# Kernel optimization log

Measured on AMD Instinct MI355X. Metric: run time of the kernel, lower is better.

The kernel has to match this reference:

```python
import jax, jax.numpy as jnp
import numpy as np

B, T, C, H, W = 2, 8, 512, 32, 32
HEADS, HD = 8, 64          # head_dim = C // num_heads
GROUPS = 32                # GroupNorm_0 num_groups
EPS = 1e-6


def setup_inputs() -> dict:
    key = jax.random.key(0)
    k = jax.random.split(key, 5)
    return {
        "x": jax.random.normal(k[0], (B, T, C, H, W), jnp.float32),
        "gn_scale": jnp.ones((C,), jnp.float32),
        "gn_bias": jnp.zeros((C,), jnp.float32),
        "w_qkv": jax.random.normal(k[1], (C, 3 * C), jnp.float32) / float(np.sqrt(C)),
        "b_qkv": jnp.zeros((3 * C,), jnp.float32),
        "w_out": jax.random.normal(k[2], (C, C), jnp.float32) / float(np.sqrt(C)),
        "b_out": jnp.zeros((C,), jnp.float32),
    }


def reference(x, gn_scale, gn_bias, w_qkv, b_qkv, w_out, b_out):
    Bv, Tv, Cv, Hv, Wv = x.shape
    N = Bv * Tv
    xv = x.reshape(N, Cv, Hv, Wv)

    # GroupNorm(32 groups, eps=1e-6) with affine
    g = xv.reshape(N, GROUPS, Cv // GROUPS, Hv, Wv)
    mu = g.mean(axis=(2, 3, 4), keepdims=True)
    var = g.var(axis=(2, 3, 4), keepdims=True)
    hn = ((g - mu) * jax.lax.rsqrt(var + EPS)).reshape(N, Cv, Hv, Wv)
    hn = hn * gn_scale[None, :, None, None] + gn_bias[None, :, None, None]

    # NIN qkv projection (per-pixel 1x1): (N,C,H,W) x (C,3C) -> (N,3C,H,W)
    h = jnp.einsum('nchw,cd->ndhw', hn, w_qkv) + b_qkv[None, :, None, None]
    h = h.reshape(N, HEADS, 3 * HD, Hv * Wv).transpose(0, 1, 3, 2)  # (N,h,S,3d)
    q, k, v = jnp.split(h, 3, axis=-1)

    # naive scaled dot-product attention over S = H*W tokens
    logits = jnp.einsum('nhsd,nhtd->nhst', q, k) / float(np.sqrt(HD))
    attn = jax.nn.softmax(logits, axis=-1)
    vals = jnp.einsum('nhst,nhtd->nhsd', attn, v)

    h = vals.transpose(0, 1, 3, 2).reshape(N, Cv, Hv, Wv)
    # output NIN (init_scale=0 in torch; random params here) + residual
    h = jnp.einsum('nchw,cd->ndhw', h, w_out) + b_out[None, :, None, None]
    return x + h.reshape(Bv, Tv, Cv, Hv, Wv)
```

## Files before the change

kernel.cpp:

```cpp
#include <hip/hip_runtime.h>
#include <stdint.h>

typedef __bf16 bf16x8 __attribute__((ext_vector_type(8)));
typedef float f32x4v __attribute__((ext_vector_type(4)));
typedef float f32x16v __attribute__((ext_vector_type(16)));
typedef unsigned u32x2 __attribute__((ext_vector_type(2)));

__device__ __forceinline__ unsigned f2bf_rn(float f) {
    return (__float_as_uint(f) + 0x8000u) >> 16;
}
__device__ __forceinline__ unsigned pk2bf(float a, float b) {
    return __builtin_amdgcn_perm(__float_as_uint(b) + 0x8000u,
                                 __float_as_uint(a) + 0x8000u, 0x07060302u);
}
__device__ __forceinline__ unsigned pk2bf_rne(float a, float b) {
    union { __bf16 h[2]; unsigned u; } x;
    x.h[0] = (__bf16)a; x.h[1] = (__bf16)b;
    return x.u;
}
__device__ __forceinline__ float fexp2(float x) {
#if __has_builtin(__builtin_amdgcn_exp2f)
    return __builtin_amdgcn_exp2f(x);
#else
    float r; asm volatile("v_exp_f32 %0, %1" : "=v"(r) : "v"(x)); return r;
#endif
}
__device__ __forceinline__ float frcp(float x) {
#if __has_builtin(__builtin_amdgcn_rcpf)
    return __builtin_amdgcn_rcpf(x);
#else
    float r; asm volatile("v_rcp_f32 %0, %1" : "=v"(r) : "v"(x)); return r;
#endif
}

__device__ __forceinline__ void swap32(unsigned &a, unsigned &b) {
#if __has_builtin(__builtin_amdgcn_permlane32_swap)
    u32x2 r = __builtin_amdgcn_permlane32_swap(a, b, false, false);
    a = r[0]; b = r[1];
#else
    unsigned pa = (unsigned)__shfl_xor((int)a, 32);
    unsigned pb = (unsigned)__shfl_xor((int)b, 32);
    bool hi = (threadIdx.x & 32) != 0;
    unsigned na = hi ? pb : a;
    unsigned nb = hi ? b : pa;
    a = na; b = nb;
#endif
}

__device__ __forceinline__ bf16x8 mk8(unsigned a, unsigned b, unsigned c, unsigned e) {
    union { int4 i; bf16x8 v; } u;
    u.i = make_int4((int)a, (int)b, (int)c, (int)e);
    return u.v;
}

#define GLD_LDS16(gp, lp) __builtin_amdgcn_global_load_lds( \
    (const __attribute__((address_space(1))) unsigned int*)(gp), \
    (__attribute__((address_space(3))) unsigned int*)(lp), 16, 0, 0)

__global__ __launch_bounds__(256) void wt_kernel(const float* __restrict__ wqkv,
        const float* __restrict__ wout, unsigned short* __restrict__ WqT,
        unsigned short* __restrict__ WoT) {
    __shared__ float tile[32][33];
    int bx = blockIdx.x;
    const float* in; unsigned short* out; int Cc, c0;
    if (bx < 48) { in = wqkv; out = WqT; Cc = 1536; c0 = bx * 32; }
    else         { in = wout; out = WoT; Cc = 512;  c0 = (bx - 48) * 32; }
    int r0 = blockIdx.y * 32;
    int tx = threadIdx.x & 31, ty = threadIdx.x >> 5;
    #pragma unroll
    for (int i = 0; i < 4; i++) {
        int r = ty + i * 8;
        tile[r][tx] = in[(size_t)(r0 + r) * Cc + c0 + tx];
    }
    __syncthreads();
    #pragma unroll
    for (int i = 0; i < 4; i++) {
        int cr = ty + i * 8;
        out[(size_t)(c0 + cr) * 512 + r0 + tx] = (unsigned short)f2bf_rn(tile[tx][cr]);
    }
}

__global__ __launch_bounds__(256) void gn_kernel(const float* __restrict__ x,
        const float* __restrict__ scale, const float* __restrict__ bias,
        unsigned short* __restrict__ hnT) {
    int blk = blockIdx.x;
    int tid = threadIdx.x;
    int g = blk & 31, n = blk >> 5;
    const float4* src4 = (const float4*)(x + (size_t)blk * 16384);

    __shared__ float xs[16][1028];
    float s = 0.f, s2 = 0.f;
    #pragma unroll
    for (int k = 0; k < 16; k++) {
        int i = tid + k * 256;
        float4 v = src4[i];
        int c = i >> 8, p4 = (i & 255) * 4;
        *(float4*)&xs[c][p4] = v;
        s  += v.x + v.y + v.z + v.w;
        s2 += v.x*v.x + v.y*v.y + v.z*v.z + v.w*v.w;
    }
    __shared__ float red[256], red2[256];
    red[tid] = s; red2[tid] = s2;
    __syncthreads();
    for (int off = 128; off > 0; off >>= 1) {
        if (tid < off) { red[tid] += red[tid+off]; red2[tid] += red2[tid+off]; }
        __syncthreads();
    }
    __shared__ float sc_s[16], bi_s[16];
    if (tid < 16) {
        float mean = red[0] * (1.f/16384.f);
        float var  = red2[0] * (1.f/16384.f) - mean*mean;
        float rstd = rsqrtf(var + 1e-6f);
        int c = g*16 + tid;
        float sc = scale[c] * rstd;
        sc_s[tid] = sc;
        bi_s[tid] = bias[c] - mean * sc;
    }
    __syncthreads();
    #pragma unroll
    for (int ch = 0; ch < 4; ch++) {
        int sQ = ch*256 + tid;
        unsigned int pk[8];
        #pragma unroll
        for (int c2 = 0; c2 < 8; c2++) {
            float a = xs[c2*2][sQ]   * sc_s[c2*2]   + bi_s[c2*2];
            float b = xs[c2*2+1][sQ] * sc_s[c2*2+1] + bi_s[c2*2+1];
            pk[c2] = pk2bf(a, b);
        }
        unsigned short* op = hnT + ((size_t)(n*1024 + sQ))*512 + g*16;
        *(uint4*)op       = make_uint4(pk[0], pk[1], pk[2], pk[3]);
        *((uint4*)op + 1) = make_uint4(pk[4], pk[5], pk[6], pk[7]);
    }
}

__global__ __launch_bounds__(256) void qkv_kernel(
        const unsigned short* __restrict__ WqT, const unsigned short* __restrict__ hnT,
        const float* __restrict__ bqkv,
        unsigned short* __restrict__ qb, unsigned short* __restrict__ kbuf,
        unsigned short* __restrict__ vb) {
    int s0 = blockIdx.x * 128, m0 = blockIdx.y * 128, n = blockIdx.z;
    __shared__ unsigned short At[8192];
    __shared__ unsigned short Bt[8192];
    int tid = threadIdx.x;
    int lane = tid & 63, w = tid >> 6;
    int quad = lane >> 4, tx = lane & 15;
    int moff = (w & 1) * 64, soff = (w >> 1) * 64;

    const unsigned short* Arow = WqT + (size_t)m0 * 512;
    const unsigned short* Brow = hnT + ((size_t)n * 1024 + s0) * 512;

    f32x4v acc[4][4];
    #pragma unroll
    for (int i = 0; i < 4; i++)
        #pragma unroll
        for (int j = 0; j < 4; j++)
            #pragma unroll
            for (int e = 0; e < 4; e++) acc[i][j][e] = 0.f;

    int f1 = tid, f2 = tid + 256;
    int m1 = f1 >> 2, kb1 = ((f1 & 3) - (f1 >> 3)) & 3;
    int m2 = f2 >> 2, kb2 = ((f2 & 3) - (f2 >> 3)) & 3;

    for (int k0 = 0; k0 < 512; k0 += 64) {
        __syncthreads();
        GLD_LDS16(Arow + (size_t)m1*512 + k0 + kb1*8,      At + f1*8);
        GLD_LDS16(Arow + (size_t)m2*512 + k0 + kb2*8,      At + f2*8);
        GLD_LDS16(Arow + (size_t)m1*512 + k0 + 32 + kb1*8, At + 4096 + f1*8);
        GLD_LDS16(Arow + (size_t)m2*512 + k0 + 32 + kb2*8, At + 4096 + f2*8);
        GLD_LDS16(Brow + (size_t)m1*512 + k0 + kb1*8,      Bt + f1*8);
        GLD_LDS16(Brow + (size_t)m2*512 + k0 + kb2*8,      Bt + f2*8);
        GLD_LDS16(Brow + (size_t)m1*512 + k0 + 32 + kb1*8, Bt + 4096 + f1*8);
        GLD_LDS16(Brow + (size_t)m2*512 + k0 + 32 + kb2*8, Bt + 4096 + f2*8);
        __syncthreads();
        #pragma unroll
        for (int kk = 0; kk < 2; kk++) {
            const unsigned short* Ab = At + kk*4096;
            const unsigned short* Bb = Bt + kk*4096;
            bf16x8 af[4], bfr[4];
            #pragma unroll
            for (int mt = 0; mt < 4; mt++) {
                int m = moff + mt*16 + tx;
                int ch = m*4 + ((quad + (m >> 1)) & 3);
                af[mt] = *(const bf16x8*)(Ab + ch*8);
            }
            #pragma unroll
            for (int nt = 0; nt < 4; nt++) {
                int m = soff + nt*16 + tx;
                int ch = m*4 + ((quad + (m >> 1)) & 3);
                bfr[nt] = *(const bf16x8*)(Bb + ch*8);
            }
            #pragma unroll
            for (int mt = 0; mt < 4; mt++)
                #pragma unroll
                for (int nt = 0; nt < 4; nt++)
                    acc[mt][nt] = __builtin_amdgcn_mfma_f32_16x16x32_bf16(
                        af[mt], bfr[nt], acc[mt][nt], 0, 0, 0);
        }
    }

    const float QSCL = 0.18033688011112042f;
    #pragma unroll
    for (int mt = 0; mt < 4; mt++) {
        int m = m0 + moff + mt*16 + quad*4;
        int head = m / 192;
        int r = m - head*192;
        int which = r >> 6;
        int d0 = r & 63;
        float4 bia = *(const float4*)(bqkv + m);
        float scl = (which == 0) ? QSCL : 1.0f;
        #pragma unroll
        for (int nt = 0; nt < 4; nt++) {
            int sQ = s0 + soff + nt*16 + tx;
            f32x4v a = acc[mt][nt];
            float v0 = (a[0]+bia.x)*scl, v1 = (a[1]+bia.y)*scl;
            float v2 = (a[2]+bia.z)*scl, v3 = (a[3]+bia.w)*scl;
            if (which < 2) {
                unsigned short* base = (which == 0) ? qb : kbuf;
                unsigned lo = pk2bf(v0, v1), hi2 = pk2bf(v2, v3);
                *(uint2*)(base + (((size_t)(n*8 + head)*1024 + sQ) << 6) + d0) =
                    make_uint2(lo, hi2);
            } else {
                size_t vbase = ((size_t)(n*8 + head)*64 + d0)*1024 + sQ;
                vb[vbase]        = (unsigned short)f2bf_rn(v0);
                vb[vbase + 1024] = (unsigned short)f2bf_rn(v1);
                vb[vbase + 2048] = (unsigned short)f2bf_rn(v2);
                vb[vbase + 3072] = (unsigned short)f2bf_rn(v3);
            }
        }
    }
}

__global__ __launch_bounds__(256) void attn_kernel(
        const unsigned short* __restrict__ qg, const unsigned short* __restrict__ kg,
        const unsigned short* __restrict__ vg, unsigned short* __restrict__ ao) {
    int bid = blockIdx.x;
    int nh = bid & 127, qbk = bid >> 7;
    int tid = threadIdx.x, w = tid >> 6, lane = tid & 63;
    int lq = lane & 31, hi = lane >> 5;
    const unsigned short* Q = qg + (size_t)nh * 65536;
    const unsigned short* K = kg + (size_t)nh * 65536;
    const unsigned short* V = vg + (size_t)nh * 65536;

    __shared__ unsigned short Klds[2][64*72];
    __shared__ unsigned short Vlds[2][64*72];

    int q0 = qbk*128 + w*32;
    bf16x8 qf[4];
    #pragma unroll
    for (int ks = 0; ks < 4; ks++)
        qf[ks] = *(const bf16x8*)(Q + ((size_t)(q0 + lq))*64 + ks*16 + hi*8);

    int r = tid >> 2, part = (tid & 3) * 16;
    uint4 ka, kb2, va, vb2;
    ka  = *(const uint4*)(K + (size_t)r*64 + part);
    kb2 = *(const uint4*)(K + (size_t)r*64 + part + 8);
    va  = *(const uint4*)(V + (size_t)r*1024 + part);
    vb2 = *(const uint4*)(V + (size_t)r*1024 + part + 8);

    const bf16x8 ONES = mk8(0x3f803f80u, 0x3f803f80u, 0x3f803f80u, 0x3f803f80u);

    f32x16v O0, O1, Os, ZED;
    #pragma unroll
    for (int i = 0; i < 16; i++) { O0[i] = 0.f; O1[i] = 0.f; Os[i] = 0.f; ZED[i] = 0.f; }

    for (int it = 0; it < 16; it++) {
        int buf = it & 1;
        {
            unsigned short* kd = Klds[buf] + r*72 + part;
            *(uint4*)kd = ka; *(uint4*)(kd+8) = kb2;
            unsigned short* vd = Vlds[buf] + r*72 + part;
            *(uint4*)vd = va; *(uint4*)(vd+8) = vb2;
        }
        __syncthreads();
        if (it < 15) {
            int t0 = (it + 1) * 64;
            ka  = *(const uint4*)(K + (size_t)(t0 + r)*64 + part);
            kb2 = *(const uint4*)(K + (size_t)(t0 + r)*64 + part + 8);
            va  = *(const uint4*)(V + (size_t)r*1024 + t0 + part);
            vb2 = *(const uint4*)(V + (size_t)r*1024 + t0 + part + 8);
        }
        const unsigned short* Kb = Klds[buf];
        const unsigned short* Vb = Vlds[buf];

        f32x16v S0, S1;
        {
            bf16x8 a0 = *(const bf16x8*)(Kb + lq*72 + hi*8);
            bf16x8 a1 = *(const bf16x8*)(Kb + (32+lq)*72 + hi*8);
            S0 = __builtin_amdgcn_mfma_f32_32x32x16_bf16(a0, qf[0], ZED, 0, 0, 0);
            S1 = __builtin_amdgcn_mfma_f32_32x32x16_bf16(a1, qf[0], ZED, 0, 0, 0);
        }
        #pragma unroll
        for (int ks = 1; ks < 4; ks++) {
            bf16x8 a0 = *(const bf16x8*)(Kb + lq*72 + ks*16 + hi*8);
            bf16x8 a1 = *(const bf16x8*)(Kb + (32+lq)*72 + ks*16 + hi*8);
            S0 = __builtin_amdgcn_mfma_f32_32x32x16_bf16(a0, qf[ks], S0, 0, 0, 0);
            S1 = __builtin_amdgcn_mfma_f32_32x32x16_bf16(a1, qf[ks], S1, 0, 0, 0);
        }

        #pragma unroll
        for (int i = 0; i < 16; i++) {
            S0[i] = fexp2(S0[i]);
            S1[i] = fexp2(S1[i]);
        }
        unsigned d[16];
        #pragma unroll
        for (int p2 = 0; p2 < 8; p2++) {
            d[p2]     = pk2bf_rne(S0[p2*2], S0[p2*2+1]);
            d[8 + p2] = pk2bf_rne(S1[p2*2], S1[p2*2+1]);
        }
        swap32(d[0],  d[2]);  swap32(d[1],  d[3]);
        swap32(d[4],  d[6]);  swap32(d[5],  d[7]);
        swap32(d[8],  d[10]); swap32(d[9],  d[11]);
        swap32(d[12], d[14]); swap32(d[13], d[15]);

        #pragma unroll
        for (int kc = 0; kc < 4; kc++) {
            bf16x8 pa = mk8(d[kc*4+0], d[kc*4+1], d[kc*4+2], d[kc*4+3]);
            bf16x8 v0 = *(const bf16x8*)(Vb + lq*72 + kc*16 + hi*8);
            bf16x8 v1 = *(const bf16x8*)(Vb + (32+lq)*72 + kc*16 + hi*8);
            O0 = __builtin_amdgcn_mfma_f32_32x32x16_bf16(pa, v0, O0, 0, 0, 0);
            O1 = __builtin_amdgcn_mfma_f32_32x32x16_bf16(pa, v1, O1, 0, 0, 0);
            Os = __builtin_amdgcn_mfma_f32_32x32x16_bf16(pa, ONES, Os, 0, 0, 0);
        }
    }

    int n = nh >> 3, h = nh & 7;
    #pragma unroll
    for (int rq = 0; rq < 4; rq++) {
        #pragma unroll
        for (int i = 0; i < 4; i++) {
            int reg = rq*4 + i;
            int sQ = q0 + rq*8 + hi*4 + i;
            float inv = frcp(Os[reg]);
            size_t rowb = ((size_t)(n*1024 + sQ))*512 + h*64;
            ao[rowb + lq]      = (unsigned short)f2bf_rn(O0[reg] * inv);
            ao[rowb + 32 + lq] = (unsigned short)f2bf_rn(O1[reg] * inv);
        }
    }
}

__global__ __launch_bounds__(256) void out_kernel(
        const unsigned short* __restrict__ aoT, const unsigned short* __restrict__ WoT,
        const float* __restrict__ bout, const float* __restrict__ x,
        float* __restrict__ out) {
    int s0 = blockIdx.x * 128, d0b = blockIdx.y * 128, n = blockIdx.z;
    __shared__ unsigned short At[8192];
    __shared__ unsigned short Bt[8192];
    int tid = threadIdx.x;
    int lane = tid & 63, w = tid >> 6;
    int quad = lane >> 4, tx = lane & 15;
    int moff = (w & 1) * 64, noff = (w >> 1) * 64;

    const unsigned short* Arow = aoT + ((size_t)n * 1024 + s0) * 512;
    const unsigned short* Brow = WoT + (size_t)d0b * 512;

    f32x4v acc[4][4];
    #pragma unroll
    for (int i = 0; i < 4; i++)
        #pragma unroll
        for (int j = 0; j < 4; j++)
            #pragma unroll
            for (int e = 0; e < 4; e++) acc[i][j][e] = 0.f;

    int f1 = tid, f2 = tid + 256;
    int m1 = f1 >> 2, kb1 = ((f1 & 3) - (f1 >> 3)) & 3;
    int m2 = f2 >> 2, kb2 = ((f2 & 3) - (f2 >> 3)) & 3;

    for (int k0 = 0; k0 < 512; k0 += 64) {
        __syncthreads();
        GLD_LDS16(Arow + (size_t)m1*512 + k0 + kb1*8,      At + f1*8);
        GLD_LDS16(Arow + (size_t)m2*512 + k0 + kb2*8,      At + f2*8);
        GLD_LDS16(Arow + (size_t)m1*512 + k0 + 32 + kb1*8, At + 4096 + f1*8);
        GLD_LDS16(Arow + (size_t)m2*512 + k0 + 32 + kb2*8, At + 4096 + f2*8);
        GLD_LDS16(Brow + (size_t)m1*512 + k0 + kb1*8,      Bt + f1*8);
        GLD_LDS16(Brow + (size_t)m2*512 + k0 + kb2*8,      Bt + f2*8);
        GLD_LDS16(Brow + (size_t)m1*512 + k0 + 32 + kb1*8, Bt + 4096 + f1*8);
        GLD_LDS16(Brow + (size_t)m2*512 + k0 + 32 + kb2*8, Bt + 4096 + f2*8);
        __syncthreads();
        #pragma unroll
        for (int kk = 0; kk < 2; kk++) {
            const unsigned short* Ab = At + kk*4096;
            const unsigned short* Bb = Bt + kk*4096;
            bf16x8 af[4], bfr[4];
            #pragma unroll
            for (int mt = 0; mt < 4; mt++) {
                int m = moff + mt*16 + tx;
                int ch = m*4 + ((quad + (m >> 1)) & 3);
                af[mt] = *(const bf16x8*)(Ab + ch*8);
            }
            #pragma unroll
            for (int nt = 0; nt < 4; nt++) {
                int m = noff + nt*16 + tx;
                int ch = m*4 + ((quad + (m >> 1)) & 3);
                bfr[nt] = *(const bf16x8*)(Bb + ch*8);
            }
            #pragma unroll
            for (int mt = 0; mt < 4; mt++)
                #pragma unroll
                for (int nt = 0; nt < 4; nt++)
                    acc[mt][nt] = __builtin_amdgcn_mfma_f32_16x16x32_bf16(
                        af[mt], bfr[nt], acc[mt][nt], 0, 0, 0);
        }
    }

    #pragma unroll
    for (int mt = 0; mt < 4; mt++) {
        int sQ = s0 + moff + mt*16 + quad*4;
        #pragma unroll
        for (int nt = 0; nt < 4; nt++) {
            int d = d0b + noff + nt*16 + tx;
            float bo = bout[d];
            size_t base = ((size_t)n*512 + d)*1024 + sQ;
            float4 xv = *(const float4*)(x + base);
            f32x4v a = acc[mt][nt];
            float4 o = make_float4(a[0]+bo+xv.x, a[1]+bo+xv.y, a[2]+bo+xv.z, a[3]+bo+xv.w);
            *(float4*)(out + base) = o;
        }
    }
}

extern "C" void kernel_launch(void* const* d_in, const int* in_sizes, int n_in,
                              void* d_out, int out_size, void* d_ws, size_t ws_size,
                              hipStream_t stream) {
    const float* x    = (const float*)d_in[0];
    const float* gns  = (const float*)d_in[1];
    const float* gnb  = (const float*)d_in[2];
    const float* wqkv = (const float*)d_in[3];
    const float* bqkv = (const float*)d_in[4];
    const float* wout = (const float*)d_in[5];
    const float* bout = (const float*)d_in[6];
    float* out = (float*)d_out;

    char* p = (char*)d_ws;
    size_t off = 0;
    auto carve = [&](size_t bytes) {
        char* r = p + off;
        off = (off + bytes + 255) & ~(size_t)255;
        return r;
    };
    unsigned short* hnT = (unsigned short*)carve((size_t)16*1024*512*2);
    unsigned short* qb2 = (unsigned short*)carve((size_t)128*1024*64*2);
    unsigned short* kb2 = (unsigned short*)carve((size_t)128*1024*64*2);
    unsigned short* vb2 = (unsigned short*)carve((size_t)128*64*1024*2);
    unsigned short* aoT = (unsigned short*)carve((size_t)16*1024*512*2);
    unsigned short* WqT = (unsigned short*)carve((size_t)1536*512*2);
    unsigned short* WoT = (unsigned short*)carve((size_t)512*512*2);

    wt_kernel<<<dim3(64, 16), 256, 0, stream>>>(wqkv, wout, WqT, WoT);
    gn_kernel<<<dim3(512), 256, 0, stream>>>(x, gns, gnb, hnT);
    qkv_kernel<<<dim3(8, 12, 16), 256, 0, stream>>>(WqT, hnT, bqkv, qb2, kb2, vb2);
    attn_kernel<<<dim3(1024), 256, 0, stream>>>(qb2, kb2, vb2, aoT);
    out_kernel<<<dim3(8, 4, 16), 256, 0, stream>>>(aoT, WoT, bout, x, out);
}
```

Measured before the change: 206.1 us.

## Process 64 query rows per wave in attention to reuse K/V tiles

Each attention wave now handles two 32-row query tiles instead of one, so every K and V fragment read from LDS feeds twice as many MFMAs, and the grid is halved to 512 blocks. The global K/V traffic per query is halved as well. s_setprio is raised around the MFMA phases to favour matrix issue across waves. The cost is much higher register pressure from doubled accumulators (launch bounds ask for 2 blocks per SM) and fewer blocks to fill the GPU.

```diff
diff --git a/kernel.cpp b/kernel.cpp
--- a/kernel.cpp
+++ b/kernel.cpp
@@ -230,7 +230,7 @@
     }
 }
 
-__global__ __launch_bounds__(256) void attn_kernel(
+__global__ __launch_bounds__(256, 2) void attn_kernel(
         const unsigned short* __restrict__ qg, const unsigned short* __restrict__ kg,
         const unsigned short* __restrict__ vg, unsigned short* __restrict__ ao) {
     int bid = blockIdx.x;
@@ -244,11 +244,13 @@
     __shared__ unsigned short Klds[2][64*72];
     __shared__ unsigned short Vlds[2][64*72];
 
-    int q0 = qbk*128 + w*32;
-    bf16x8 qf[4];
-    #pragma unroll
-    for (int ks = 0; ks < 4; ks++)
-        qf[ks] = *(const bf16x8*)(Q + ((size_t)(q0 + lq))*64 + ks*16 + hi*8);
+    int q0 = qbk*256 + w*64;
+    bf16x8 qfA[4], qfB[4];
+    #pragma unroll
+    for (int ks = 0; ks < 4; ks++) {
+        qfA[ks] = *(const bf16x8*)(Q + ((size_t)(q0 + lq))*64 + ks*16 + hi*8);
+        qfB[ks] = *(const bf16x8*)(Q + ((size_t)(q0 + 32 + lq))*64 + ks*16 + hi*8);
+    }
 
     int r = tid >> 2, part = (tid & 3) * 16;
     uint4 ka, kb2, va, vb2;
@@ -259,9 +261,12 @@
 
     const bf16x8 ONES = mk8(0x3f803f80u, 0x3f803f80u, 0x3f803f80u, 0x3f803f80u);
 
-    f32x16v O0, O1, Os, ZED;
-    #pragma unroll
-    for (int i = 0; i < 16; i++) { O0[i] = 0.f; O1[i] = 0.f; Os[i] = 0.f; ZED[i] = 0.f; }
+    f32x16v O0a, O1a, O0b, O1b, Osa, Osb, ZED;
+    #pragma unroll
+    for (int i = 0; i < 16; i++) {
+        O0a[i] = 0.f; O1a[i] = 0.f; O0b[i] = 0.f; O1b[i] = 0.f;
+        Osa[i] = 0.f; Osb[i] = 0.f; ZED[i] = 0.f;
+    }
 
     for (int it = 0; it < 16; it++) {
         int buf = it & 1;
@@ -282,46 +287,74 @@
         const unsigned short* Kb = Klds[buf];
         const unsigned short* Vb = Vlds[buf];
 
-        f32x16v S0, S1;
+        f32x16v S0, S1, U0, U1;
+        __builtin_amdgcn_s_setprio(1);
         {
             bf16x8 a0 = *(const bf16x8*)(Kb + lq*72 + hi*8);
             bf16x8 a1 = *(const bf16x8*)(Kb + (32+lq)*72 + hi*8);
-            S0 = __builtin_amdgcn_mfma_f32_32x32x16_bf16(a0, qf[0], ZED, 0, 0, 0);
-            S1 = __builtin_amdgcn_mfma_f32_32x32x16_bf16(a1, qf[0], ZED, 0, 0, 0);
+            S0 = __builtin_amdgcn_mfma_f32_32x32x16_bf16(a0, qfA[0], ZED, 0, 0, 0);
+            S1 = __builtin_amdgcn_mfma_f32_32x32x16_bf16(a1, qfA[0], ZED, 0, 0, 0);
+            U0 = __builtin_amdgcn_mfma_f32_32x32x16_bf16(a0, qfB[0], ZED, 0, 0, 0);
+            U1 = __builtin_amdgcn_mfma_f32_32x32x16_bf16(a1, qfB[0], ZED, 0, 0, 0);
         }
         #pragma unroll
         for (int ks = 1; ks < 4; ks++) {
             bf16x8 a0 = *(const bf16x8*)(Kb + lq*72 + ks*16 + hi*8);
             bf16x8 a1 = *(const bf16x8*)(Kb + (32+lq)*72 + ks*16 + hi*8);
-            S0 = __builtin_amdgcn_mfma_f32_32x32x16_bf16(a0, qf[ks], S0, 0, 0, 0);
-            S1 = __builtin_amdgcn_mfma_f32_32x32x16_bf16(a1, qf[ks], S1, 0, 0, 0);
-        }
+            S0 = __builtin_amdgcn_mfma_f32_32x32x16_bf16(a0, qfA[ks], S0, 0, 0, 0);
+            S1 = __builtin_amdgcn_mfma_f32_32x32x16_bf16(a1, qfA[ks], S1, 0, 0, 0);
+            U0 = __builtin_amdgcn_mfma_f32_32x32x16_bf16(a0, qfB[ks], U0, 0, 0, 0);
+            U1 = __builtin_amdgcn_mfma_f32_32x32x16_bf16(a1, qfB[ks], U1, 0, 0, 0);
+        }
+        __builtin_amdgcn_s_setprio(0);
 
         #pragma unroll
         for (int i = 0; i < 16; i++) {
             S0[i] = fexp2(S0[i]);
             S1[i] = fexp2(S1[i]);
         }
-        unsigned d[16];
+        unsigned dA[16];
         #pragma unroll
         for (int p2 = 0; p2 < 8; p2++) {
-            d[p2]     = pk2bf_rne(S0[p2*2], S0[p2*2+1]);
-            d[8 + p2] = pk2bf_rne(S1[p2*2], S1[p2*2+1]);
-        }
-        swap32(d[0],  d[2]);  swap32(d[1],  d[3]);
-        swap32(d[4],  d[6]);  swap32(d[5],  d[7]);
-        swap32(d[8],  d[10]); swap32(d[9],  d[11]);
-        swap32(d[12], d[14]); swap32(d[13], d[15]);
-
+            dA[p2]     = pk2bf_rne(S0[p2*2], S0[p2*2+1]);
+            dA[8 + p2] = pk2bf_rne(S1[p2*2], S1[p2*2+1]);
+        }
+        swap32(dA[0],  dA[2]);  swap32(dA[1],  dA[3]);
+        swap32(dA[4],  dA[6]);  swap32(dA[5],  dA[7]);
+        swap32(dA[8],  dA[10]); swap32(dA[9],  dA[11]);
+        swap32(dA[12], dA[14]); swap32(dA[13], dA[15]);
+
+        #pragma unroll
+        for (int i = 0; i < 16; i++) {
+            U0[i] = fexp2(U0[i]);
+            U1[i] = fexp2(U1[i]);
+        }
+        unsigned dB[16];
+        #pragma unroll
+        for (int p2 = 0; p2 < 8; p2++) {
+            dB[p2]     = pk2bf_rne(U0[p2*2], U0[p2*2+1]);
+            dB[8 + p2] = pk2bf_rne(U1[p2*2], U1[p2*2+1]);
+        }
+        swap32(dB[0],  dB[2]);  swap32(dB[1],  dB[3]);
+        swap32(dB[4],  dB[6]);  swap32(dB[5],  dB[7]);
+        swap32(dB[8],  dB[10]); swap32(dB[9],  dB[11]);
+        swap32(dB[12], dB[14]); swap32(dB[13], dB[15]);
+
+        __builtin_amdgcn_s_setprio(1);
         #pragma unroll
         for (int kc = 0; kc < 4; kc++) {
-            bf16x8 pa = mk8(d[kc*4+0], d[kc*4+1], d[kc*4+2], d[kc*4+3]);
+            bf16x8 paA = mk8(dA[kc*4+0], dA[kc*4+1], dA[kc*4+2], dA[kc*4+3]);
+            bf16x8 paB = mk8(dB[kc*4+0], dB[kc*4+1], dB[kc*4+2], dB[kc*4+3]);
             bf16x8 v0 = *(const bf16x8*)(Vb + lq*72 + kc*16 + hi*8);
             bf16x8 v1 = *(const bf16x8*)(Vb + (32+lq)*72 + kc*16 + hi*8);
-            O0 = __builtin_amdgcn_mfma_f32_32x32x16_bf16(pa, v0, O0, 0, 0, 0);
-            O1 = __builtin_amdgcn_mfma_f32_32x32x16_bf16(pa, v1, O1, 0, 0, 0);
-            Os = __builtin_amdgcn_mfma_f32_32x32x16_bf16(pa, ONES, Os, 0, 0, 0);
-        }
+            O0a = __builtin_amdgcn_mfma_f32_32x32x16_bf16(paA, v0, O0a, 0, 0, 0);
+            O1a = __builtin_amdgcn_mfma_f32_32x32x16_bf16(paA, v1, O1a, 0, 0, 0);
+            O0b = __builtin_amdgcn_mfma_f32_32x32x16_bf16(paB, v0, O0b, 0, 0, 0);
+            O1b = __builtin_amdgcn_mfma_f32_32x32x16_bf16(paB, v1, O1b, 0, 0, 0);
+            Osa = __builtin_amdgcn_mfma_f32_32x32x16_bf16(paA, ONES, Osa, 0, 0, 0);
+            Osb = __builtin_amdgcn_mfma_f32_32x32x16_bf16(paB, ONES, Osb, 0, 0, 0);
+        }
+        __builtin_amdgcn_s_setprio(0);
     }
 
     int n = nh >> 3, h = nh & 7;
@@ -331,10 +364,14 @@
         for (int i = 0; i < 4; i++) {
             int reg = rq*4 + i;
             int sQ = q0 + rq*8 + hi*4 + i;
-            float inv = frcp(Os[reg]);
-            size_t rowb = ((size_t)(n*1024 + sQ))*512 + h*64;
-            ao[rowb + lq]      = (unsigned short)f2bf_rn(O0[reg] * inv);
-            ao[rowb + 32 + lq] = (unsigned short)f2bf_rn(O1[reg] * inv);
+            float invA = frcp(Osa[reg]);
+            float invB = frcp(Osb[reg]);
+            size_t rowbA = ((size_t)(n*1024 + sQ))*512 + h*64;
+            size_t rowbB = ((size_t)(n*1024 + sQ + 32))*512 + h*64;
+            ao[rowbA + lq]      = (unsigned short)f2bf_rn(O0a[reg] * invA);
+            ao[rowbA + 32 + lq] = (unsigned short)f2bf_rn(O1a[reg] * invA);
+            ao[rowbB + lq]      = (unsigned short)f2bf_rn(O0b[reg] * invB);
+            ao[rowbB + 32 + lq] = (unsigned short)f2bf_rn(O1b[reg] * invB);
         }
     }
 }
@@ -449,6 +486,6 @@
     wt_kernel<<<dim3(64, 16), 256, 0, stream>>>(wqkv, wout, WqT, WoT);
     gn_kernel<<<dim3(512), 256, 0, stream>>>(x, gns, gnb, hnT);
     qkv_kernel<<<dim3(8, 12, 16), 256, 0, stream>>>(WqT, hnT, bqkv, qb2, kb2, vb2);
-    attn_kernel<<<dim3(1024), 256, 0, stream>>>(qb2, kb2, vb2, aoT);
+    attn_kernel<<<dim3(512), 256, 0, stream>>>(qb2, kb2, vb2, aoT);
     out_kernel<<<dim3(8, 4, 16), 256, 0, stream>>>(aoT, WoT, bout, x, out);
 }
```

New measurement: 198.0 us. -3.9%, faster.
